# Kernel optimization log

Hardware: AMD Instinct MI355X
Metric: run time of the kernel (lower is better)

The kernel has to match this reference:

```python
import jax, jax.numpy as jnp
import numpy as np

DIM = 1024
N_HEADS = 16
HEAD_DIM = DIM // N_HEADS
MLP_DIM = 4096
B, L, M = 4, 1024, 1024
EPS = 1e-5


def _mha(q_in, k_in, v_in, mask, wq, wk, wv, wo):
    b, l, d = q_in.shape
    m = k_in.shape[1]
    # torch view(b, l, head_dim, n_heads): split last dim as (head_dim, n_heads)
    q = (q_in @ wq).reshape(b, l, HEAD_DIM, N_HEADS)
    k = (k_in @ wk).reshape(b, m, HEAD_DIM, N_HEADS)
    v = (v_in @ wv).reshape(b, m, HEAD_DIM, N_HEADS)  # computed but unused downstream (source quirk)
    score = jnp.einsum('bldn,bmdn->blmn', q, k)
    # source applies mask BEFORE scaling
    score = jnp.where(mask, jnp.float32(-1e9), score)
    score = score / (HEAD_DIM ** 0.5)
    attn = jax.nn.softmax(score, axis=2)
    # SOURCE QUIRK: second einsum uses k, not v — reproduced faithfully
    x = jnp.einsum('blmn,bmdn->bldn', attn, k)
    x = x.reshape(b, l, d)  # 'b l d n -> b l (d n)'
    return x @ wo


def _layer_norm(x, g, b):
    mu = jnp.mean(x, axis=-1, keepdims=True)
    var = jnp.var(x, axis=-1, keepdims=True)
    return (x - mu) * jax.lax.rsqrt(var + EPS) * g + b


def setup_inputs() -> dict:
    key = jax.random.key(0)
    ks = jax.random.split(key, 16)
    s = 0.02
    inp = {
        'x': jax.random.normal(ks[0], (B, L, DIM), dtype=jnp.float32),
        'enc_output': jax.random.normal(ks[1], (B, M, DIM), dtype=jnp.float32),
        # causal mask: True above diagonal => masked
        'self_attn_mask': jnp.triu(jnp.ones((L, L), dtype=bool), k=1)[None, :, :, None],
        'enc_dec_mask': jnp.zeros((1, L, M, 1), dtype=bool),
        'sa_wq': s * jax.random.normal(ks[2], (DIM, DIM), jnp.float32),
        'sa_wk': s * jax.random.normal(ks[3], (DIM, DIM), jnp.float32),
        'sa_wv': s * jax.random.normal(ks[4], (DIM, DIM), jnp.float32),
        'sa_wo': s * jax.random.normal(ks[5], (DIM, DIM), jnp.float32),
        'ca_wq': s * jax.random.normal(ks[6], (DIM, DIM), jnp.float32),
        'ca_wk': s * jax.random.normal(ks[7], (DIM, DIM), jnp.float32),
        'ca_wv': s * jax.random.normal(ks[8], (DIM, DIM), jnp.float32),
        'ca_wo': s * jax.random.normal(ks[9], (DIM, DIM), jnp.float32),
        'ln1_g': jnp.ones((DIM,), jnp.float32), 'ln1_b': jnp.zeros((DIM,), jnp.float32),
        'ln2_g': jnp.ones((DIM,), jnp.float32), 'ln2_b': jnp.zeros((DIM,), jnp.float32),
        'ln3_g': jnp.ones((DIM,), jnp.float32), 'ln3_b': jnp.zeros((DIM,), jnp.float32),
        'ff_w1': s * jax.random.normal(ks[10], (DIM, MLP_DIM), jnp.float32),
        'ff_b1': jnp.zeros((MLP_DIM,), jnp.float32),
        'ff_w2': s * jax.random.normal(ks[11], (MLP_DIM, DIM), jnp.float32),
        'ff_b2': jnp.zeros((DIM,), jnp.float32),
    }
    return inp


def reference(x, enc_output, self_attn_mask, enc_dec_mask,
              sa_wq, sa_wk, sa_wv, sa_wo,
              ca_wq, ca_wk, ca_wv, ca_wo,
              ln1_g, ln1_b, ln2_g, ln2_b, ln3_g, ln3_b,
              ff_w1, ff_b1, ff_w2, ff_b2):
    # self-attention + residual + LN (dropout = identity in eval)
    h = x + _mha(x, x, x, self_attn_mask, sa_wq, sa_wk, sa_wv, sa_wo)
    h = _layer_norm(h, ln1_g, ln1_b)
    # encoder-decoder attention + residual + LN
    h = h + _mha(h, enc_output, enc_output, enc_dec_mask, ca_wq, ca_wk, ca_wv, ca_wo)
    h = _layer_norm(h, ln2_g, ln2_b)
    # position-wise FFN (gelu, exact erf like torch default) + residual + LN
    ff = jax.nn.gelu(h @ ff_w1 + ff_b1, approximate=False) @ ff_w2 + ff_b2
    h = h + ff
    h = _layer_norm(h, ln3_g, ln3_b)
    return h
```

## Files before the change

### kernel.cpp

```cpp
#include <hip/hip_runtime.h>
#include <hip/hip_bf16.h>
#include <stdint.h>

typedef unsigned short u16;
typedef _Float16 f16x8 __attribute__((ext_vector_type(8)));
typedef float f32x4 __attribute__((ext_vector_type(4)));

#define TOK 4096

__device__ __forceinline__ u16 f2h(float f) {
  _Float16 h = (_Float16)f;
  return __builtin_bit_cast(unsigned short, h);
}
__device__ __forceinline__ float h2f(u16 b) {
  return (float)__builtin_bit_cast(_Float16, b);
}
__device__ __forceinline__ unsigned pack2(float a, float b) {
  return (unsigned)f2h(a) | ((unsigned)f2h(b) << 16);
}
__device__ __forceinline__ void gld16(const u16* g, u16* l) {
  __builtin_amdgcn_global_load_lds(
      (const __attribute__((address_space(1))) void*)g,
      (__attribute__((address_space(3))) void*)l, 16, 0, 0);
}
__device__ __forceinline__ float gelu_fast(float v) {
  float z = 1.5957691216f * v * (1.0f + 0.044715f * v * v);
  return v / (1.0f + __expf(-z));
}

__device__ __forceinline__ void tc_body(const float* W, u16* Wt, int K, int N,
                                        int bx, int by, int tid) {
  __shared__ float tile[32][33];
  int n0 = bx * 32, k0 = by * 32;
  int tx = tid & 31, ty = tid >> 5;
#pragma unroll
  for (int e = 0; e < 4; e++)
    tile[ty + e * 8][tx] = W[(size_t)(k0 + ty + e * 8) * N + n0 + tx];
  __syncthreads();
#pragma unroll
  for (int e = 0; e < 4; e++)
    Wt[(size_t)(n0 + ty + e * 8) * K + k0 + tx] = f2h(tile[tx][ty + e * 8]);
}
__device__ __forceinline__ void cast_body(const float* in, u16* out, int blk, int tid) {
  int i = blk * 256 + tid;
  const float4* p = (const float4*)(in + (size_t)i * 8);
  float4 a = p[0], b = p[1];
  uint4 o;
  o.x = pack2(a.x, a.y); o.y = pack2(a.z, a.w);
  o.z = pack2(b.x, b.y); o.w = pack2(b.z, b.w);
  *(uint4*)(out + (size_t)i * 8) = o;
}

__global__ __launch_bounds__(256) void prep_kernel(
    const float* x, const float* enc, u16* xh, u16* ench,
    const float* W0, const float* W1, const float* W2,
    const float* W3, const float* W4, const float* W5,
    u16* T0, u16* T1, u16* T2, u16* T3, u16* T4, u16* T5,
    const float* Wff1, u16* Tff1, const float* Wff2, u16* Tff2) {
  int blk = blockIdx.x, tid = threadIdx.x;
  if (blk < 2048) { cast_body(x, xh, blk, tid); return; }
  if (blk < 4096) { cast_body(enc, ench, blk - 2048, tid); return; }
  if (blk < 10240) {
    int t = blk - 4096;
    int z = t >> 10, s = t & 1023;
    const float* W; u16* T;
    switch (z) {
      case 0: W = W0; T = T0; break;
      case 1: W = W1; T = T1; break;
      case 2: W = W2; T = T2; break;
      case 3: W = W3; T = T3; break;
      case 4: W = W4; T = T4; break;
      default: W = W5; T = T5; break;
    }
    tc_body(W, T, 1024, 1024, s & 31, s >> 5, tid);
    return;
  }
  if (blk < 14336) {
    int t = blk - 10240;
    tc_body(Wff1, Tff1, 1024, 4096, t & 127, t >> 7, tid);
    return;
  }
  {
    int t = blk - 14336;
    tc_body(Wff2, Tff2, 4096, 1024, t & 31, t >> 5, tid);
  }
}

template <int EPI, int BN, int BK>
__global__ __launch_bounds__((BN == 256) ? 512 : 256)
void gemm_bt_kernel(const u16* __restrict__ A0,
                    const u16* __restrict__ A1,
                    const u16* __restrict__ Bt,
                    u16* __restrict__ Cb0,
                    u16* __restrict__ Cb1,
                    u16* __restrict__ CbT,
                    const float* __restrict__ bias,
                    int M, int N, int K, int KLEN) {
  constexpr int SWM = BK / 8 - 1;
  __shared__ u16 As[2][128 * BK];
  __shared__ u16 Bs[2][BN * BK];
  int tid = threadIdx.x, lane = tid & 63, wid = tid >> 6;
  int gx = gridDim.x, gy = gridDim.y;
  int nwg = gx * gy;
  int flat = blockIdx.x + gx * blockIdx.y;
  int k8 = flat & 7, idx = flat >> 3;
  int bx, by;
  if (gx >= 16) {
    int rx = gx >> 2, ry = gy >> 1;
    int kx = k8 & 3, ky = k8 >> 2;
    bx = kx * rx + idx % rx;
    by = ky * ry + idx / rx;
  } else {
    int widx = k8 * (nwg >> 3) + idx;
    bx = widx % gx;
    by = widx / gx;
  }
  int row0 = by * 128, col0 = bx * BN;
  bool is_k = (EPI == 0) && (col0 >= 1024);
  const u16* A = is_k ? A1 : A0;
  int wm = (BN == 256) ? (wid >> 2) * 64 : (wid >> 1) * 64;
  int wn = (BN == 256) ? (wid & 3) * 64 : (wid & 1) * 64;
  size_t koff = (EPI == 4) ? (size_t)blockIdx.z * KLEN : 0;
  int ra = lane & 15, kg = lane >> 4;

  const u16 *Ab0, *Ab1, *Bb0, *Bb1;
  if constexpr (BK == 64) {
    int srow = wid * 8 + (lane >> 3);
    int ssw = (lane & 7) ^ ((srow >> 1) & 7);
    Ab0 = A + (size_t)(row0 + srow) * K + koff + ssw * 8;
    Bb0 = Bt + (size_t)(col0 + srow) * K + koff + ssw * 8;
    Ab1 = nullptr; Bb1 = nullptr;
  } else {
    int sr = tid >> 2;
    int scol = (((tid & 3) ^ ((sr >> 1) & 3)) * 8);
    Ab0 = A + (size_t)(row0 + sr) * K + koff + scol;
    Ab1 = A + (size_t)(row0 + 64 + sr) * K + koff + scol;
    Bb0 = Bt + (size_t)(col0 + sr) * K + koff + scol;
    Bb1 = Bt + (size_t)(col0 + ((BN == 256) ? 128 : 64) + sr) * K + koff + scol;
  }

  f32x4 acc[4][4];
#pragma unroll
  for (int i = 0; i < 4; i++)
#pragma unroll
    for (int j = 0; j < 4; j++) { acc[i][j][0] = 0.f; acc[i][j][1] = 0.f; acc[i][j][2] = 0.f; acc[i][j][3] = 0.f; }
  int KT = KLEN / BK;
  int arow[4], asw[4], brow[4], bsw[4];
#pragma unroll
  for (int i = 0; i < 4; i++) {
    arow[i] = wm + i * 16 + ra;
    asw[i] = (arow[i] >> 1) & SWM;
    brow[i] = wn + i * 16 + ra;
    bsw[i] = (brow[i] >> 1) & SWM;
  }

  auto STAGE = [&](int kt, int buf) {
    if constexpr (BK == 64) {
#pragma unroll
      for (int i = 0; i < 4; i++) {
        gld16(Ab0 + (size_t)i * 32 * K + kt * 64, &As[buf][i * 2048 + wid * 512]);
        gld16(Bb0 + (size_t)i * 32 * K + kt * 64, &Bs[buf][i * 2048 + wid * 512]);
      }
    } else if constexpr (BN == 256) {
      gld16(Ab0 + kt * 32, &As[buf][wid * 512]);
      gld16(Bb0 + kt * 32, &Bs[buf][wid * 512]);
      gld16(Bb1 + kt * 32, &Bs[buf][4096 + wid * 512]);
    } else {
      gld16(Ab0 + kt * 32, &As[buf][wid * 512]);
      gld16(Ab1 + kt * 32, &As[buf][2048 + wid * 512]);
      gld16(Bb0 + kt * 32, &Bs[buf][wid * 512]);
      gld16(Bb1 + kt * 32, &Bs[buf][2048 + wid * 512]);
    }
  };

  STAGE(0, 0);
  __syncthreads();
  int cur = 0;
  for (int kt = 0; kt < KT; ++kt) {
    if (kt + 1 < KT) STAGE(kt + 1, cur ^ 1);
#pragma unroll
    for (int kk = 0; kk < BK / 32; kk++) {
      f16x8 af[4], bfv[4];
#pragma unroll
      for (int i = 0; i < 4; i++)
        af[i] = *(const f16x8*)&As[cur][arow[i] * BK + (((kk * 4 + kg) ^ asw[i]) * 8)];
#pragma unroll
      for (int j = 0; j < 4; j++)
        bfv[j] = *(const f16x8*)&Bs[cur][brow[j] * BK + (((kk * 4 + kg) ^ bsw[j]) * 8)];
#pragma unroll
      for (int i = 0; i < 4; i++)
#pragma unroll
        for (int j = 0; j < 4; j++)
          acc[i][j] = __builtin_amdgcn_mfma_f32_16x16x32_f16(af[i], bfv[j], acc[i][j], 0, 0, 0);
    }
    __syncthreads();
    cur ^= 1;
  }

  int rq = kg * 4;
#pragma unroll
  for (int i = 0; i < 4; i++) {
    int rowb = row0 + wm + i * 16 + rq;
    if (EPI == 0) {
      int b = rowb >> 10, l0 = rowb & 1023;
      int d0 = ((col0 + wn) >> 4) & 63;
      size_t hb = ((size_t)(b * 16 + ra)) * 1024;
      u16* dst = is_k ? Cb1 : Cb0;
      u16 h[4][4];
#pragma unroll
      for (int j = 0; j < 4; j++)
#pragma unroll
        for (int q = 0; q < 4; q++) h[j][q] = f2h(acc[i][j][q]);
#pragma unroll
      for (int q = 0; q < 4; q++) {
        ushort4 hv;
        hv.x = h[0][q]; hv.y = h[1][q]; hv.z = h[2][q]; hv.w = h[3][q];
        *(ushort4*)&dst[(hb + l0 + q) * 64 + d0] = hv;
      }
      if (is_k) {
#pragma unroll
        for (int j = 0; j < 4; j++) {
          uint2 ov;
          ov.x = (unsigned)h[j][0] | ((unsigned)h[j][1] << 16);
          ov.y = (unsigned)h[j][2] | ((unsigned)h[j][3] << 16);
          *(uint2*)&CbT[((size_t)(b * 16 + ra)) * 65536 + ((size_t)(d0 + j)) * 1024 + l0] = ov;
        }
      }
    } else {
#pragma unroll
      for (int j = 0; j < 4; j++) {
        int col = col0 + wn + j * 16 + ra;
        float bval = 0.f;
        if (EPI == 2) bval = bias[col];
        if (EPI == 4 && blockIdx.z == 0 && bias) bval = bias[col];
#pragma unroll
        for (int q = 0; q < 4; q++) {
          int row = rowb + q;
          float v = acc[i][j][q] + bval;
          if (EPI == 2) {
            Cb0[(size_t)row * N + col] = f2h(gelu_fast(v));
          } else {
            Cb0[(size_t)blockIdx.z * M * N + (size_t)row * N + col] = f2h(v);
          }
        }
      }
    }
  }
}

template <bool CAUSAL>
__global__ __launch_bounds__(512) void flash4_kernel(const u16* __restrict__ Qh,
                                                     const u16* __restrict__ Kh,
                                                     const u16* __restrict__ KhT,
                                                     u16* __restrict__ Xtok) {
  const int L = 1024;
  int tid = threadIdx.x, lane = tid & 63, wid = tid >> 6;
  int flat = blockIdx.x + 8 * blockIdx.y;
  int xcd = flat & 7, idx = flat >> 3;
  int slot = idx >> 5, j_ = idx & 31;
  int q2 = j_ & 3;
  int qt = CAUSAL ? (slot ? 7 - q2 : q2) : (slot * 4 + q2);
  int bh = xcd * 8 + (j_ >> 2);
  __shared__ u16 Ks[2][4096];
  __shared__ u16 Kt[2][4096];
  __shared__ u16 Ps[8][1024];
  int ra = lane & 15, kg = lane >> 4, rq = kg * 4;
  int wr0 = qt * 128 + wid * 16;
  f16x8 qa0, qa1;
  {
    const u16* Qb = Qh + ((size_t)bh * L + wr0 + ra) * 64;
    qa0 = *(const f16x8*)(Qb + kg * 8);
    qa1 = *(const f16x8*)(Qb + 32 + kg * 8);
  }
  f32x4 oacc[4];
#pragma unroll
  for (int d = 0; d < 4; d++) { oacc[d][0] = 0.f; oacc[d][1] = 0.f; oacc[d][2] = 0.f; oacc[d][3] = 0.f; }
  float l_acc[4] = {0.f, 0.f, 0.f, 0.f};
  int ntiles = CAUSAL ? (2 * qt + 2) : 16;
  int fr = lane >> 3, fc = lane & 7;
  int rr = wid * 8 + fr;
  int cc_ = fc ^ (rr & 7);
  int sw = ra & 7;

#define KSTAGE(mt, buf) do {                                                            \
    gld16(Kh + ((size_t)bh * L + (mt) * 64 + rr) * 64 + cc_ * 8, &Ks[buf][wid * 512]);  \
    gld16(KhT + ((size_t)bh * 64 + rr) * L + (size_t)(mt) * 64 + cc_ * 8, &Kt[buf][wid * 512]); \
  } while (0)

  KSTAGE(0, 0);
  __syncthreads();
  int cur = 0;
  for (int mt = 0; mt < ntiles; ++mt) {
    if (mt + 1 < ntiles) KSTAGE(mt + 1, cur ^ 1);
    bool active = !(CAUSAL && (wr0 + 15 < mt * 64));
    if (active) {
      bool wmask = CAUSAL && (mt * 64 + 63 > wr0);
      float p[4][4];
      __builtin_amdgcn_s_setprio(1);
#pragma unroll
      for (int j = 0; j < 4; j++) {
        int krow = j * 16 + ra;
        f16x8 kb0 = *(const f16x8*)&Ks[cur][krow * 64 + ((kg ^ sw) * 8)];
        f16x8 kb1 = *(const f16x8*)&Ks[cur][krow * 64 + (((4 + kg) ^ sw) * 8)];
        f32x4 a; a[0] = 0.f; a[1] = 0.f; a[2] = 0.f; a[3] = 0.f;
        a = __builtin_amdgcn_mfma_f32_16x16x32_f16(qa0, kb0, a, 0, 0, 0);
        a = __builtin_amdgcn_mfma_f32_16x16x32_f16(qa1, kb1, a, 0, 0, 0);
#pragma unroll
        for (int q = 0; q < 4; q++) {
          float v = a[q] * 0.125f;
          if (wmask) {
            int rg = wr0 + rq + q;
            int cg = mt * 64 + j * 16 + ra;
            if (cg > rg) v = -1.25e8f;
          }
          p[j][q] = __expf(v);
        }
      }
      __builtin_amdgcn_s_setprio(0);
#pragma unroll
      for (int q = 0; q < 4; q++)
        l_acc[q] += (p[0][q] + p[1][q]) + (p[2][q] + p[3][q]);
#pragma unroll
      for (int j = 0; j < 4; j++)
#pragma unroll
        for (int q = 0; q < 4; q++) {
          int prow = rq + q;
          int pcol = j * 16 + ra;
          Ps[wid][prow * 64 + (((pcol >> 3) ^ (prow & 7)) * 8) + (pcol & 7)] = f2h(p[j][q]);
        }
      f16x8 pa0 = *(const f16x8*)&Ps[wid][ra * 64 + ((kg ^ sw) * 8)];
      f16x8 pa1 = *(const f16x8*)&Ps[wid][ra * 64 + (((4 + kg) ^ sw) * 8)];
      __builtin_amdgcn_s_setprio(1);
#pragma unroll
      for (int d = 0; d < 4; d++) {
        int krow = d * 16 + ra;
        f16x8 kc0 = *(const f16x8*)&Kt[cur][krow * 64 + ((kg ^ sw) * 8)];
        f16x8 kc1 = *(const f16x8*)&Kt[cur][krow * 64 + (((4 + kg) ^ sw) * 8)];
        oacc[d] = __builtin_amdgcn_mfma_f32_16x16x32_f16(pa0, kc0, oacc[d], 0, 0, 0);
        oacc[d] = __builtin_amdgcn_mfma_f32_16x16x32_f16(pa1, kc1, oacc[d], 0, 0, 0);
      }
      __builtin_amdgcn_s_setprio(0);
    }
    __syncthreads();
    cur ^= 1;
  }
#undef KSTAGE
#pragma unroll
  for (int off = 1; off < 16; off <<= 1)
#pragma unroll
    for (int q = 0; q < 4; q++) l_acc[q] += __shfl_xor(l_acc[q], off);
  int b = bh >> 4, nh = bh & 15;
#pragma unroll
  for (int q = 0; q < 4; q++) {
    float inv = 1.0f / l_acc[q];
    int l = wr0 + rq + q;
    size_t rowg = ((size_t)b * 1024 + l) * 1024;
#pragma unroll
    for (int d = 0; d < 4; d++)
      Xtok[rowg + (d * 16 + ra) * 16 + nh] = f2h(oacc[d][q] * inv);
  }
}

template <int WRITE_F, int P>
__global__ __launch_bounds__(256) void ln_kernel(const u16* __restrict__ parts,
                                                 const u16* __restrict__ res,
                                                 const float* __restrict__ g,
                                                 const float* __restrict__ bb,
                                                 float* __restrict__ outf,
                                                 u16* __restrict__ outh) {
  int row = blockIdx.x, tid = threadIdx.x;
  int lane = tid & 63, wid = tid >> 6;
  size_t base = (size_t)row * 1024 + tid * 4;
  uint2 vr = *(const uint2*)&res[base];
  float x0 = h2f((u16)vr.x), x1 = h2f((u16)(vr.x >> 16));
  float x2 = h2f((u16)vr.y), x3 = h2f((u16)(vr.y >> 16));
#pragma unroll
  for (int p = 0; p < P; p++) {
    uint2 v = *(const uint2*)&parts[(size_t)p * 4194304 + base];
    x0 += h2f((u16)v.x);
    x1 += h2f((u16)(v.x >> 16));
    x2 += h2f((u16)v.y);
    x3 += h2f((u16)(v.y >> 16));
  }
  float s = x0 + x1 + x2 + x3;
  float sq = x0 * x0 + x1 * x1 + x2 * x2 + x3 * x3;
#pragma unroll
  for (int off = 1; off < 64; off <<= 1) {
    s += __shfl_xor(s, off);
    sq += __shfl_xor(sq, off);
  }
  __shared__ float red[8];
  if (lane == 0) { red[wid] = s; red[4 + wid] = sq; }
  __syncthreads();
  s = red[0] + red[1] + red[2] + red[3];
  sq = red[4] + red[5] + red[6] + red[7];
  float mean = s * (1.0f / 1024.0f);
  float var = sq * (1.0f / 1024.0f) - mean * mean;
  float rstd = rsqrtf(var + 1e-5f);
  float4 vg = *(const float4*)(g + tid * 4);
  float4 vb = *(const float4*)(bb + tid * 4);
  float y0 = (x0 - mean) * rstd * vg.x + vb.x;
  float y1 = (x1 - mean) * rstd * vg.y + vb.y;
  float y2 = (x2 - mean) * rstd * vg.z + vb.z;
  float y3 = (x3 - mean) * rstd * vg.w + vb.w;
  if (WRITE_F) {
    float4 yo; yo.x = y0; yo.y = y1; yo.z = y2; yo.w = y3;
    *(float4*)(outf + base) = yo;
  } else {
    uint2 ov; ov.x = pack2(y0, y1); ov.y = pack2(y2, y3);
    *(uint2*)(outh + base) = ov;
  }
}

extern "C" void kernel_launch(void* const* d_in, const int* in_sizes, int n_in,
                              void* d_out, int out_size, void* d_ws, size_t ws_size,
                              hipStream_t stream) {
  (void)in_sizes; (void)n_in; (void)out_size; (void)ws_size;
  const float* x    = (const float*)d_in[0];
  const float* enc  = (const float*)d_in[1];
  const float* sa_wq = (const float*)d_in[4];
  const float* sa_wk = (const float*)d_in[5];
  const float* sa_wo = (const float*)d_in[7];
  const float* ca_wq = (const float*)d_in[8];
  const float* ca_wk = (const float*)d_in[9];
  const float* ca_wo = (const float*)d_in[11];
  const float* ln1g = (const float*)d_in[12];
  const float* ln1b = (const float*)d_in[13];
  const float* ln2g = (const float*)d_in[14];
  const float* ln2b = (const float*)d_in[15];
  const float* ln3g = (const float*)d_in[16];
  const float* ln3b = (const float*)d_in[17];
  const float* ffw1 = (const float*)d_in[18];
  const float* ffb1 = (const float*)d_in[19];
  const float* ffw2 = (const float*)d_in[20];
  const float* ffb2 = (const float*)d_in[21];

  uint8_t* w = (uint8_t*)d_ws;
  const size_t MB = 1024ull * 1024ull;
  u16* wt_saqk = (u16*)(w + 0 * MB);
  u16* wt_sao  = (u16*)(w + 4 * MB);
  u16* wt_caqk = (u16*)(w + 6 * MB);
  u16* wt_cao  = (u16*)(w + 10 * MB);
  u16* wt_ff1  = (u16*)(w + 12 * MB);
  u16* wt_ff2  = (u16*)(w + 20 * MB);
  u16* act_h   = (u16*)(w + 28 * MB);
  u16* enc_h   = (u16*)(w + 36 * MB);
  u16* qhd     = (u16*)(w + 44 * MB);
  u16* khd     = (u16*)(w + 52 * MB);
  u16* khdT    = (u16*)(w + 60 * MB);
  u16* ctxtok  = (u16*)(w + 68 * MB);
  u16* parts   = (u16*)(w + 76 * MB);
  u16* ff1h = qhd;

  prep_kernel<<<18432, 256, 0, stream>>>(
      x, enc, act_h, enc_h,
      sa_wq, sa_wk, sa_wo, ca_wq, ca_wk, ca_wo,
      wt_saqk, wt_saqk + 1024 * 1024, wt_sao,
      wt_caqk, wt_caqk + 1024 * 1024, wt_cao,
      ffw1, wt_ff1, ffw2, wt_ff2);

  gemm_bt_kernel<0, 128, 64><<<dim3(16, 32, 1), 256, 0, stream>>>(
      act_h, act_h, wt_saqk, qhd, khd, khdT, nullptr, TOK, 2048, 1024, 1024);
  flash4_kernel<true><<<dim3(8, 64), 512, 0, stream>>>(qhd, khd, khdT, ctxtok);
  gemm_bt_kernel<4, 128, 64><<<dim3(8, 32, 2), 256, 0, stream>>>(
      ctxtok, ctxtok, wt_sao, parts, nullptr, nullptr, nullptr, TOK, 1024, 1024, 512);
  ln_kernel<0, 2><<<4096, 256, 0, stream>>>(parts, act_h, ln1g, ln1b, nullptr, act_h);

  gemm_bt_kernel<0, 128, 64><<<dim3(16, 32, 1), 256, 0, stream>>>(
      act_h, enc_h, wt_caqk, qhd, khd, khdT, nullptr, TOK, 2048, 1024, 1024);
  flash4_kernel<false><<<dim3(8, 64), 512, 0, stream>>>(qhd, khd, khdT, ctxtok);
  gemm_bt_kernel<4, 128, 64><<<dim3(8, 32, 2), 256, 0, stream>>>(
      ctxtok, ctxtok, wt_cao, parts, nullptr, nullptr, nullptr, TOK, 1024, 1024, 512);
  ln_kernel<0, 2><<<4096, 256, 0, stream>>>(parts, act_h, ln2g, ln2b, nullptr, act_h);

  gemm_bt_kernel<2, 256, 32><<<dim3(16, 32, 1), 512, 0, stream>>>(
      act_h, act_h, wt_ff1, ff1h, nullptr, nullptr, ffb1, TOK, 4096, 1024, 1024);
  gemm_bt_kernel<4, 128, 64><<<dim3(8, 32, 2), 256, 0, stream>>>(
      ff1h, ff1h, wt_ff2, parts, nullptr, nullptr, ffb2, TOK, 1024, 4096, 2048);
  ln_kernel<1, 2><<<4096, 256, 0, stream>>>(parts, act_h, ln3g, ln3b, (float*)d_out, nullptr);
}
```

Before: 298.5 us.

## Switch GEMM to triple-buffered BK=32 pipeline with explicit vmcnt waits

Replaces the double-buffered GEMM, which used BK=64 for most calls, with a three-stage ring of BK=32 LDS buffers. Loads are issued two tiles ahead and completion is tracked with explicit s_waitcnt vmcnt counts and raw s_barrier plus sched_barrier, instead of __syncthreads. The goal is to keep more global-to-LDS loads in flight and hide memory latency behind the MFMAs. In exchange, each barrier now covers only 16 MFMAs for the BK=64 users, and the hand-written vmcnt counts must match exactly how many loads each stage issues.

```diff
diff --git a/kernel.cpp b/kernel.cpp
--- a/kernel.cpp
+++ b/kernel.cpp
@@ -86,7 +86,7 @@
   }
 }
 
-template <int EPI, int BN, int BK>
+template <int EPI, int BN>
 __global__ __launch_bounds__((BN == 256) ? 512 : 256)
 void gemm_bt_kernel(const u16* __restrict__ A0,
                     const u16* __restrict__ A1,
@@ -96,9 +96,9 @@
                     u16* __restrict__ CbT,
                     const float* __restrict__ bias,
                     int M, int N, int K, int KLEN) {
-  constexpr int SWM = BK / 8 - 1;
-  __shared__ u16 As[2][128 * BK];
-  __shared__ u16 Bs[2][BN * BK];
+  constexpr int NLOADS = (BN == 256) ? 3 : 4;
+  __shared__ u16 As[3][128 * 32];
+  __shared__ u16 Bs[3][BN * 32];
   int tid = threadIdx.x, lane = tid & 63, wid = tid >> 6;
   int gx = gridDim.x, gy = gridDim.y;
   int nwg = gx * gy;
@@ -123,45 +123,30 @@
   size_t koff = (EPI == 4) ? (size_t)blockIdx.z * KLEN : 0;
   int ra = lane & 15, kg = lane >> 4;
 
-  const u16 *Ab0, *Ab1, *Bb0, *Bb1;
-  if constexpr (BK == 64) {
-    int srow = wid * 8 + (lane >> 3);
-    int ssw = (lane & 7) ^ ((srow >> 1) & 7);
-    Ab0 = A + (size_t)(row0 + srow) * K + koff + ssw * 8;
-    Bb0 = Bt + (size_t)(col0 + srow) * K + koff + ssw * 8;
-    Ab1 = nullptr; Bb1 = nullptr;
-  } else {
-    int sr = tid >> 2;
-    int scol = (((tid & 3) ^ ((sr >> 1) & 3)) * 8);
-    Ab0 = A + (size_t)(row0 + sr) * K + koff + scol;
-    Ab1 = A + (size_t)(row0 + 64 + sr) * K + koff + scol;
-    Bb0 = Bt + (size_t)(col0 + sr) * K + koff + scol;
-    Bb1 = Bt + (size_t)(col0 + ((BN == 256) ? 128 : 64) + sr) * K + koff + scol;
-  }
+  int sr = tid >> 2;
+  int scol = (((tid & 3) ^ ((sr >> 1) & 3)) * 8);
+  const u16* Ab0 = A + (size_t)(row0 + sr) * K + koff + scol;
+  const u16* Ab1 = A + (size_t)(row0 + 64 + sr) * K + koff + scol;
+  const u16* Bb0 = Bt + (size_t)(col0 + sr) * K + koff + scol;
+  const u16* Bb1 = Bt + (size_t)(col0 + ((BN == 256) ? 128 : 64) + sr) * K + koff + scol;
 
   f32x4 acc[4][4];
 #pragma unroll
   for (int i = 0; i < 4; i++)
 #pragma unroll
     for (int j = 0; j < 4; j++) { acc[i][j][0] = 0.f; acc[i][j][1] = 0.f; acc[i][j][2] = 0.f; acc[i][j][3] = 0.f; }
-  int KT = KLEN / BK;
+  int KT = KLEN >> 5;
   int arow[4], asw[4], brow[4], bsw[4];
 #pragma unroll
   for (int i = 0; i < 4; i++) {
     arow[i] = wm + i * 16 + ra;
-    asw[i] = (arow[i] >> 1) & SWM;
+    asw[i] = (arow[i] >> 1) & 3;
     brow[i] = wn + i * 16 + ra;
-    bsw[i] = (brow[i] >> 1) & SWM;
+    bsw[i] = (brow[i] >> 1) & 3;
   }
 
   auto STAGE = [&](int kt, int buf) {
-    if constexpr (BK == 64) {
-#pragma unroll
-      for (int i = 0; i < 4; i++) {
-        gld16(Ab0 + (size_t)i * 32 * K + kt * 64, &As[buf][i * 2048 + wid * 512]);
-        gld16(Bb0 + (size_t)i * 32 * K + kt * 64, &Bs[buf][i * 2048 + wid * 512]);
-      }
-    } else if constexpr (BN == 256) {
+    if constexpr (BN == 256) {
       gld16(Ab0 + kt * 32, &As[buf][wid * 512]);
       gld16(Bb0 + kt * 32, &Bs[buf][wid * 512]);
       gld16(Bb1 + kt * 32, &Bs[buf][4096 + wid * 512]);
@@ -174,27 +159,34 @@
   };
 
   STAGE(0, 0);
-  __syncthreads();
-  int cur = 0;
+  STAGE(1, 1);
+  int cur = 0, stg = 2;
   for (int kt = 0; kt < KT; ++kt) {
-    if (kt + 1 < KT) STAGE(kt + 1, cur ^ 1);
-#pragma unroll
-    for (int kk = 0; kk < BK / 32; kk++) {
-      f16x8 af[4], bfv[4];
-#pragma unroll
-      for (int i = 0; i < 4; i++)
-        af[i] = *(const f16x8*)&As[cur][arow[i] * BK + (((kk * 4 + kg) ^ asw[i]) * 8)];
+    if (kt + 1 < KT) {
+      if constexpr (NLOADS == 3) asm volatile("s_waitcnt vmcnt(3)" ::: "memory");
+      else                       asm volatile("s_waitcnt vmcnt(4)" ::: "memory");
+    } else {
+      asm volatile("s_waitcnt vmcnt(0)" ::: "memory");
+    }
+    __builtin_amdgcn_s_barrier();
+    __builtin_amdgcn_sched_barrier(0);
+    f16x8 af[4], bfv[4];
+#pragma unroll
+    for (int i = 0; i < 4; i++)
+      af[i] = *(const f16x8*)&As[cur][arow[i] * 32 + ((kg ^ asw[i]) * 8)];
+#pragma unroll
+    for (int j = 0; j < 4; j++)
+      bfv[j] = *(const f16x8*)&Bs[cur][brow[j] * 32 + ((kg ^ bsw[j]) * 8)];
+#pragma unroll
+    for (int i = 0; i < 4; i++)
 #pragma unroll
       for (int j = 0; j < 4; j++)
-        bfv[j] = *(const f16x8*)&Bs[cur][brow[j] * BK + (((kk * 4 + kg) ^ bsw[j]) * 8)];
-#pragma unroll
-      for (int i = 0; i < 4; i++)
-#pragma unroll
-        for (int j = 0; j < 4; j++)
-          acc[i][j] = __builtin_amdgcn_mfma_f32_16x16x32_f16(af[i], bfv[j], acc[i][j], 0, 0, 0);
-    }
-    __syncthreads();
-    cur ^= 1;
+        acc[i][j] = __builtin_amdgcn_mfma_f32_16x16x32_f16(af[i], bfv[j], acc[i][j], 0, 0, 0);
+    __builtin_amdgcn_sched_barrier(0);
+    __builtin_amdgcn_s_barrier();
+    if (kt + 2 < KT) STAGE(kt + 2, stg);
+    cur = (cur == 2) ? 0 : cur + 1;
+    stg = (stg == 2) ? 0 : stg + 1;
   }
 
   int rq = kg * 4;
@@ -459,23 +451,23 @@
       wt_caqk, wt_caqk + 1024 * 1024, wt_cao,
       ffw1, wt_ff1, ffw2, wt_ff2);
 
-  gemm_bt_kernel<0, 128, 64><<<dim3(16, 32, 1), 256, 0, stream>>>(
+  gemm_bt_kernel<0, 128><<<dim3(16, 32, 1), 256, 0, stream>>>(
       act_h, act_h, wt_saqk, qhd, khd, khdT, nullptr, TOK, 2048, 1024, 1024);
   flash4_kernel<true><<<dim3(8, 64), 512, 0, stream>>>(qhd, khd, khdT, ctxtok);
-  gemm_bt_kernel<4, 128, 64><<<dim3(8, 32, 2), 256, 0, stream>>>(
+  gemm_bt_kernel<4, 128><<<dim3(8, 32, 2), 256, 0, stream>>>(
       ctxtok, ctxtok, wt_sao, parts, nullptr, nullptr, nullptr, TOK, 1024, 1024, 512);
   ln_kernel<0, 2><<<4096, 256, 0, stream>>>(parts, act_h, ln1g, ln1b, nullptr, act_h);
 
-  gemm_bt_kernel<0, 128, 64><<<dim3(16, 32, 1), 256, 0, stream>>>(
+  gemm_bt_kernel<0, 128><<<dim3(16, 32, 1), 256, 0, stream>>>(
       act_h, enc_h, wt_caqk, qhd, khd, khdT, nullptr, TOK, 2048, 1024, 1024);
   flash4_kernel<false><<<dim3(8, 64), 512, 0, stream>>>(qhd, khd, khdT, ctxtok);
-  gemm_bt_kernel<4, 128, 64><<<dim3(8, 32, 2), 256, 0, stream>>>(
+  gemm_bt_kernel<4, 128><<<dim3(8, 32, 2), 256, 0, stream>>>(
       ctxtok, ctxtok, wt_cao, parts, nullptr, nullptr, nullptr, TOK, 1024, 1024, 512);
   ln_kernel<0, 2><<<4096, 256, 0, stream>>>(parts, act_h, ln2g, ln2b, nullptr, act_h);
 
-  gemm_bt_kernel<2, 256, 32><<<dim3(16, 32, 1), 512, 0, stream>>>(
+  gemm_bt_kernel<2, 256><<<dim3(16, 32, 1), 512, 0, stream>>>(
       act_h, act_h, wt_ff1, ff1h, nullptr, nullptr, ffb1, TOK, 4096, 1024, 1024);
-  gemm_bt_kernel<4, 128, 64><<<dim3(8, 32, 2), 256, 0, stream>>>(
+  gemm_bt_kernel<4, 128><<<dim3(8, 32, 2), 256, 0, stream>>>(
       ff1h, ff1h, wt_ff2, parts, nullptr, nullptr, ffb2, TOK, 1024, 4096, 2048);
   ln_kernel<1, 2><<<4096, 256, 0, stream>>>(parts, act_h, ln3g, ln3b, (float*)d_out, nullptr);
 }
```

After: 315.1 us. 5.6% more time.
